# Kernel optimization log

Measured on AMD Instinct MI355X. Metric: run time of the kernel, lower is better.

The kernel has to match this reference:

```python
import jax, jax.numpy as jnp
import numpy as np

K_SEM = 5          # max_semantic_edges
THRESH = 0.2       # semantic_threshold
NEG_INF = -1e30


def setup_inputs() -> dict:
    key = jax.random.key(0)
    k1, k2 = jax.random.split(key)
    message_embeddings = jax.random.normal(k1, (8192, 256), dtype=jnp.float32)
    edge_emb_table = jax.random.normal(k2, (2, 64), dtype=jnp.float32)
    return {"message_embeddings": message_embeddings, "edge_emb_table": edge_emb_table}


def reference(message_embeddings, edge_emb_table):
    N = message_embeddings.shape[0]

    # ---- temporal edges: for each i -> [i,i+1] then [i+1,i] (interleaved) ----
    i = jnp.arange(N - 1)
    fwd = jnp.stack([i, i + 1])            # [2, N-1]
    bwd = jnp.stack([i + 1, i])            # [2, N-1]
    temporal = jnp.stack([fwd, bwd], axis=2).reshape(2, -1)   # [2, 2(N-1)]
    n_temporal = 2 * (N - 1)

    # ---- semantic edges: per-row top-k over sim[i, :i] with threshold ----
    norm = jnp.sqrt(jnp.sum(message_embeddings * message_embeddings, axis=1, keepdims=True))
    emb_n = message_embeddings / jnp.maximum(norm, 1e-12)     # F.normalize(p=2)
    sim = emb_n @ emb_n.T                                      # [N, N]

    r = jnp.arange(N)[:, None]
    c = jnp.arange(N)[None, :]
    # zero out diagonal and adjacent (temporal) pairs, as the torch mask does
    sim = sim * (jnp.abs(r - c) > 1)
    # restrict candidates to j < i (strictly earlier messages)
    cand = jnp.where(c < r, sim, NEG_INF)                      # [N, N]

    vals, idxs = jax.lax.top_k(cand, K_SEM)                    # [N, K]
    sem_src = idxs.reshape(-1)                                 # [N*K]
    sem_dst = jnp.repeat(jnp.arange(N), K_SEM)                 # [N*K]
    sem_valid = (vals > THRESH).reshape(-1)                    # [N*K]

    # ---- assemble padded fixed-size edge set ----
    edge_index = jnp.concatenate([temporal, jnp.stack([sem_src, sem_dst])], axis=1)
    edge_types = jnp.concatenate(
        [jnp.zeros((n_temporal,), jnp.int32), jnp.ones((N * K_SEM,), jnp.int32)])
    valid = jnp.concatenate([jnp.ones((n_temporal,), bool), sem_valid])

    edge_attr = edge_emb_table[edge_types] * valid[:, None].astype(edge_emb_table.dtype)
    edge_index = jnp.where(valid[None, :], edge_index, -1)
    return edge_index, edge_attr, valid
```

## Files before the change

kernel.cpp:

```cpp
#include <hip/hip_runtime.h>

#define N_MSG 8192
#define DIM 256
#define KS 5
#define THRESH 0.2f
#define FILT 0.196f
#define N_TEMPORAL (2*(N_MSG-1))
#define N_EDGES (N_TEMPORAL + N_MSG*KS)
#define ATTR_OFF (2*N_EDGES)
#define VALID_OFF (ATTR_OFF + N_EDGES*64)
#define BM 128
#define NTILE (N_MSG / BM)
#define NBLOCKS (NTILE*(NTILE+1)/2)
#define CAP 32

typedef __bf16 bf16x8 __attribute__((ext_vector_type(8)));
typedef __bf16 bf16x4 __attribute__((ext_vector_type(4)));
typedef float  f32x4  __attribute__((ext_vector_type(4)));

__device__ __forceinline__ void gload_lds16(const void* g, void* l) {
    __builtin_amdgcn_global_load_lds(
        (const __attribute__((address_space(1))) void*)g,
        (__attribute__((address_space(3))) void*)l, 16, 0, 0);
}

__device__ __forceinline__ void ins5(float v, int j, float (&vv)[KS], int (&xx)[KS]) {
    float cv = v; int cj = j;
#pragma unroll
    for (int k = 0; k < KS; ++k) {
        bool b = (cv > vv[k]) || (cv == vv[k] && cj < xx[k]);
        float tv = b ? vv[k] : cv; int tj = b ? xx[k] : cj;
        vv[k] = b ? cv : vv[k];    xx[k] = b ? cj : xx[k];
        cv = tv; cj = tj;
    }
}

__global__ void normalize_k(const float* __restrict__ emb, float* __restrict__ embn,
                            __bf16* __restrict__ embh, int* __restrict__ cnt) {
    int lane = threadIdx.x & 63;
    int row = blockIdx.x * 4 + (threadIdx.x >> 6);
    const float4 x = *(const float4*)(emb + (size_t)row * DIM + lane * 4);
    float ss = x.x * x.x;
    ss = fmaf(x.y, x.y, ss); ss = fmaf(x.z, x.z, ss); ss = fmaf(x.w, x.w, ss);
#pragma unroll
    for (int off = 1; off <= 32; off <<= 1) ss += __shfl_xor(ss, off);
    float nrm = fmaxf(sqrtf(ss), 1e-12f);
    float4 y; y.x = x.x / nrm; y.y = x.y / nrm; y.z = x.z / nrm; y.w = x.w / nrm;
    *(float4*)(embn + (size_t)row * DIM + lane * 4) = y;
    bf16x4 h; h[0] = (__bf16)y.x; h[1] = (__bf16)y.y; h[2] = (__bf16)y.z; h[3] = (__bf16)y.w;
    *(bf16x4*)(embh + (size_t)row * DIM + lane * 4) = h;
    if (lane == 0) cnt[row] = 0;
}

__global__ __launch_bounds__(256, 2)
void sim_filter_k(const __bf16* __restrict__ embh, int* __restrict__ cnt,
                  int* __restrict__ cidx) {
    __shared__ __align__(16) __bf16 As[BM * 128];
    __shared__ __align__(16) __bf16 Bs[BM * 128];

    int t = blockIdx.x;
    int bi = (int)((sqrtf(8.0f * (float)t + 1.0f) - 1.0f) * 0.5f);
    while ((bi + 1) * (bi + 2) / 2 <= t) ++bi;
    while (bi * (bi + 1) / 2 > t) --bi;
    int bj = t - bi * (bi + 1) / 2;
    const int i0 = bi * BM, j0 = bj * BM;

    const int tid = threadIdx.x;
    const int lane = tid & 63;
    const int ws = tid >> 6;
    const int wm = ws >> 1, wn = ws & 1;
    const int lr = lane & 15, kb = lane >> 4;

    f32x4 acc[4][4];
#pragma unroll
    for (int m = 0; m < 4; ++m)
#pragma unroll
        for (int n = 0; n < 4; ++n) { f32x4 z = {0.f, 0.f, 0.f, 0.f}; acc[m][n] = z; }

#pragma unroll
    for (int h = 0; h < 2; ++h) {
        if (h) __syncthreads();
#pragma unroll
        for (int q = 0; q < 8; ++q) {
            int g = q * 256 + tid;
            int row = g >> 4, s = g & 15;
            int sc = s ^ (row & 7);
            gload_lds16(embh + (size_t)(i0 + row) * DIM + h * 128 + sc * 8, &As[(size_t)g * 8]);
            gload_lds16(embh + (size_t)(j0 + row) * DIM + h * 128 + sc * 8, &Bs[(size_t)g * 8]);
        }
        __syncthreads();

#pragma unroll
        for (int ks = 0; ks < 4; ++ks) {
            bf16x8 a[4], b[4];
#pragma unroll
            for (int f = 0; f < 4; ++f) {
                int ra = wm * 64 + f * 16 + lr;
                a[f] = *(const bf16x8*)&As[(size_t)ra * 128 + (((ks * 4 + kb) ^ (ra & 7)) << 3)];
                int rb = wn * 64 + f * 16 + lr;
                b[f] = *(const bf16x8*)&Bs[(size_t)rb * 128 + (((ks * 4 + kb) ^ (rb & 7)) << 3)];
            }
#pragma unroll
            for (int m = 0; m < 4; ++m)
#pragma unroll
                for (int n = 0; n < 4; ++n)
                    acc[m][n] = __builtin_amdgcn_mfma_f32_16x16x32_bf16(a[m], b[n], acc[m][n], 0, 0, 0);
        }
    }

#pragma unroll
    for (int m = 0; m < 4; ++m) {
        int i = i0 + wm * 64 + m * 16 + kb * 4;
#pragma unroll
        for (int n = 0; n < 4; ++n) {
            int j = j0 + wn * 64 + n * 16 + lr;
#pragma unroll
            for (int r = 0; r < 4; ++r) {
                float v = acc[m][n][r];
                int ii = i + r;
                if (v > FILT && j <= ii - 2) {
                    int c = atomicAdd(&cnt[ii], 1);
                    if (c < CAP) cidx[(size_t)ii * CAP + c] = j;
                }
            }
        }
    }
}

template<bool FUSE>
__global__ void rescue_k(const float* __restrict__ embn, const int* __restrict__ cnt,
                         const int* __restrict__ cidx, const float* __restrict__ table,
                         float* __restrict__ out) {
    int lane = threadIdx.x & 63;
    int i = blockIdx.x * 4 + (threadIdx.x >> 6);
    int nc = cnt[i]; if (nc > CAP) nc = CAP;

    float fv[KS]; int fx[KS];
#pragma unroll
    for (int k = 0; k < KS; ++k) { fv[k] = -1e30f; fx[k] = -1; }

    if (nc > 0) {
        const float4 a = *(const float4*)(embn + (size_t)i * DIM + lane * 4);
        for (int c = 0; c < nc; ++c) {
            int j = cidx[(size_t)i * CAP + c];
            const float4 b = *(const float4*)(embn + (size_t)j * DIM + lane * 4);
            float p = a.x * b.x;
            p = fmaf(a.y, b.y, p); p = fmaf(a.z, b.z, p); p = fmaf(a.w, b.w, p);
#pragma unroll
            for (int off = 1; off <= 32; off <<= 1) p += __shfl_xor(p, off);
            if (p > THRESH) ins5(p, j, fv, fx);
        }
    }
    int vcnt = 0;
#pragma unroll
    for (int k = 0; k < KS; ++k) vcnt += (fv[k] > THRESH) ? 1 : 0;

    float tsem = FUSE ? table[64 + lane] : 0.0f;
#pragma unroll
    for (int k = 0; k < KS; ++k) {
        int e = N_TEMPORAL + i * KS + k;
        bool val = (k < vcnt);
        if (lane == 0) {
            out[e]             = val ? (float)fx[k] : -1.0f;
            out[N_EDGES + e]   = val ? (float)i     : -1.0f;
            out[VALID_OFF + e] = val ? 1.0f : 0.0f;
        }
        if (FUSE) out[ATTR_OFF + (size_t)e * 64 + lane] = val ? tsem : 0.0f;
    }
    if (FUSE) {
        if (i < N_MSG - 1) {
            float ttem = table[lane];
            int e0 = 2 * i;
            out[ATTR_OFF + (size_t)e0 * 64 + lane]       = ttem;
            out[ATTR_OFF + (size_t)(e0 + 1) * 64 + lane] = ttem;
            if (lane == 0) {
                out[e0]                 = (float)i;
                out[N_EDGES + e0]       = (float)(i + 1);
                out[VALID_OFF + e0]     = 1.0f;
                out[e0 + 1]             = (float)(i + 1);
                out[N_EDGES + e0 + 1]   = (float)i;
                out[VALID_OFF + e0 + 1] = 1.0f;
            }
        }
    }
}

__global__ void attr_out_k(const float* __restrict__ table, float* __restrict__ out) {
    int idx = blockIdx.x * 256 + threadIdx.x;
    int e = idx >> 4, sub = idx & 15;
    if (e >= N_EDGES) return;
    float4 a4;
    if (e < N_TEMPORAL) {
        a4 = *(const float4*)(table + sub * 4);
        if (sub == 0) {
            int i = e >> 1;
            out[e]             = (e & 1) ? (float)(i + 1) : (float)i;
            out[N_EDGES + e]   = (e & 1) ? (float)i       : (float)(i + 1);
            out[VALID_OFF + e] = 1.0f;
        }
    } else {
        float vld = out[VALID_OFF + e];
        a4 = *(const float4*)(table + 64 + sub * 4);
        a4.x *= vld; a4.y *= vld; a4.z *= vld; a4.w *= vld;
    }
    *(float4*)(out + ATTR_OFF + (size_t)e * 64 + sub * 4) = a4;
}

extern "C" void kernel_launch(void* const* d_in, const int* in_sizes, int n_in,
                              void* d_out, int out_size, void* d_ws, size_t ws_size,
                              hipStream_t stream) {
    const float* emb   = (const float*)d_in[0];
    const float* table = (const float*)d_in[1];
    float* out = (float*)d_out;

    size_t embn_f  = (size_t)N_MSG * DIM;
    size_t embh_f  = (size_t)N_MSG * DIM / 2;
    size_t cidx_f  = (size_t)N_MSG * CAP;
    size_t cnt_f   = N_MSG;
    size_t need_bytes = (embn_f + embh_f + cidx_f + cnt_f) * 4;

    bool have_ws = (ws_size >= need_bytes);
    float* scratch = have_ws ? (float*)d_ws
                             : out + ATTR_OFF;
    float*  embn = scratch;
    __bf16* embh = (__bf16*)(scratch + embn_f);
    int*    cidx = (int*)(scratch + embn_f + embh_f);
    int*    cnt  = (int*)(scratch + embn_f + embh_f + cidx_f);

    normalize_k<<<N_MSG / 4, 256, 0, stream>>>(emb, embn, embh, cnt);
    sim_filter_k<<<NBLOCKS, 256, 0, stream>>>(embh, cnt, cidx);
    if (have_ws) {
        rescue_k<true><<<N_MSG / 4, 256, 0, stream>>>(embn, cnt, cidx, table, out);
    } else {
        rescue_k<false><<<N_MSG / 4, 256, 0, stream>>>(embn, cnt, cidx, table, out);
        attr_out_k<<<((size_t)N_EDGES * 16 + 255) / 256, 256, 0, stream>>>(table, out);
    }
}
```

Before: 67.01 us.

## Double-buffer K-slices in sim GEMM with smaller LDS tiles for higher occupancy

Measured after the change: 92.50 us. +38.0%, slower.

```diff
diff --git a/kernel.cpp b/kernel.cpp
--- a/kernel.cpp
+++ b/kernel.cpp
@@ -52,11 +52,11 @@
     if (lane == 0) cnt[row] = 0;
 }
 
-__global__ __launch_bounds__(256, 2)
+__global__ __launch_bounds__(256, 5)
 void sim_filter_k(const __bf16* __restrict__ embh, int* __restrict__ cnt,
                   int* __restrict__ cidx) {
-    __shared__ __align__(16) __bf16 As[BM * 128];
-    __shared__ __align__(16) __bf16 Bs[BM * 128];
+    __shared__ __align__(16) __bf16 As[2][BM * 32];
+    __shared__ __align__(16) __bf16 Bs[2][BM * 32];
 
     int t = blockIdx.x;
     int bi = (int)((sqrtf(8.0f * (float)t + 1.0f) - 1.0f) * 0.5f);
@@ -71,41 +71,50 @@
     const int wm = ws >> 1, wn = ws & 1;
     const int lr = lane & 15, kb = lane >> 4;
 
+    const int gm = tid & 127;
+    const int gk1 = tid >> 7, gk2 = gk1 + 2;
+
     f32x4 acc[4][4];
 #pragma unroll
     for (int m = 0; m < 4; ++m)
 #pragma unroll
         for (int n = 0; n < 4; ++n) { f32x4 z = {0.f, 0.f, 0.f, 0.f}; acc[m][n] = z; }
 
-#pragma unroll
-    for (int h = 0; h < 2; ++h) {
-        if (h) __syncthreads();
-#pragma unroll
-        for (int q = 0; q < 8; ++q) {
-            int g = q * 256 + tid;
-            int row = g >> 4, s = g & 15;
-            int sc = s ^ (row & 7);
-            gload_lds16(embh + (size_t)(i0 + row) * DIM + h * 128 + sc * 8, &As[(size_t)g * 8]);
-            gload_lds16(embh + (size_t)(j0 + row) * DIM + h * 128 + sc * 8, &Bs[(size_t)g * 8]);
-        }
-        __syncthreads();
-
-#pragma unroll
-        for (int ks = 0; ks < 4; ++ks) {
-            bf16x8 a[4], b[4];
-#pragma unroll
-            for (int f = 0; f < 4; ++f) {
-                int ra = wm * 64 + f * 16 + lr;
-                a[f] = *(const bf16x8*)&As[(size_t)ra * 128 + (((ks * 4 + kb) ^ (ra & 7)) << 3)];
-                int rb = wn * 64 + f * 16 + lr;
-                b[f] = *(const bf16x8*)&Bs[(size_t)rb * 128 + (((ks * 4 + kb) ^ (rb & 7)) << 3)];
-            }
-#pragma unroll
-            for (int m = 0; m < 4; ++m)
-#pragma unroll
-                for (int n = 0; n < 4; ++n)
-                    acc[m][n] = __builtin_amdgcn_mfma_f32_16x16x32_bf16(a[m], b[n], acc[m][n], 0, 0, 0);
-        }
+    const __bf16* rowA = embh + (size_t)(i0 + gm) * DIM;
+    const __bf16* rowB = embh + (size_t)(j0 + gm) * DIM;
+
+    auto stage = [&](int kt, int buf) {
+        gload_lds16(rowA + kt + gk1 * 8, &As[buf][(size_t)tid * 8]);
+        gload_lds16(rowA + kt + gk2 * 8, &As[buf][((size_t)tid + 256) * 8]);
+        gload_lds16(rowB + kt + gk1 * 8, &Bs[buf][(size_t)tid * 8]);
+        gload_lds16(rowB + kt + gk2 * 8, &Bs[buf][((size_t)tid + 256) * 8]);
+    };
+
+    stage(0, 0);
+#pragma unroll
+    for (int tk = 0; tk < 8; ++tk) {
+        const int cur = tk & 1;
+        if (tk < 7) {
+            stage((tk + 1) * 32, cur ^ 1);
+            asm volatile("s_waitcnt vmcnt(4)" ::: "memory");
+        } else {
+            asm volatile("s_waitcnt vmcnt(0)" ::: "memory");
+        }
+        __builtin_amdgcn_s_barrier();
+
+        bf16x8 a[4], b[4];
+#pragma unroll
+        for (int f = 0; f < 4; ++f) {
+            a[f] = *(const bf16x8*)&As[cur][(size_t)(kb * 128 + wm * 64 + f * 16 + lr) * 8];
+            b[f] = *(const bf16x8*)&Bs[cur][(size_t)(kb * 128 + wn * 64 + f * 16 + lr) * 8];
+        }
+#pragma unroll
+        for (int m = 0; m < 4; ++m)
+#pragma unroll
+            for (int n = 0; n < 4; ++n)
+                acc[m][n] = __builtin_amdgcn_mfma_f32_16x16x32_bf16(a[m], b[n], acc[m][n], 0, 0, 0);
+
+        if (tk < 7) __builtin_amdgcn_s_barrier();
     }
 
 #pragma unroll
```
